# Performance work log

Hardware: AMD Instinct MI355X
Metric: run time of the kernel (lower is better)

## Reference

```python
import jax, jax.numpy as jnp
import numpy as np

# dims
B, S, IN, H = 8, 2048, 512, 512
# biophysical constants (from module defaults / buffers)
DT = 0.1
TAU_M, TAU_ADAPT = 20.0, 100.0
V_REST, V_THRESH, V_RESET = -65.0, -50.0, -65.0
ADAPT_A, ADAPT_B = 0.5, 0.1
E_NA, E_K, E_L = 50.0, -77.0, -54.4
# HH gate initial values (IonicCurrents lazy init)
M0, H0, N0 = 0.05, 0.6, 0.32


def setup_inputs() -> dict:
    key = jax.random.key(0)
    k1, k2 = jax.random.split(key)
    x = jax.random.normal(k1, (B, S, IN), dtype=jnp.float32)
    W = jax.random.normal(k2, (H, IN), dtype=jnp.float32) * 0.01  # SynapticPlasticity.weights
    return {
        "x": x,
        "W": W,
        "g_Na": jnp.float32(120.0),
        "g_K": jnp.float32(36.0),
        "g_L": jnp.float32(0.3),
    }


def reference(x, W, g_Na, g_K, g_L):
    """BiologicalSNNLayer.forward, first call (all internal states at init).

    post_spikes = psp0 = 0 and traces start at 0, so the STDP dw is exactly 0
    on this call; psp = 0*decay + syn_input = syn_input.
    """
    dt = jnp.float32(DT)
    # SynapticPlasticity forward output: F.linear(x, W)
    syn = jnp.einsum("bsi,hi->bsh", x, W)  # [B,S,H]
    psp = syn
    V = psp
    # Hodgkin-Huxley gating: one Euler step from initial gate values
    am = 0.1 * (V + 40.0) / (1.0 - jnp.exp(-(V + 40.0) / 10.0))
    bm = 4.0 * jnp.exp(-(V + 65.0) / 18.0)
    ah = 0.07 * jnp.exp(-(V + 65.0) / 20.0)
    bh = 1.0 / (1.0 + jnp.exp(-(V + 35.0) / 10.0))
    an = 0.01 * (V + 55.0) / (1.0 - jnp.exp(-(V + 55.0) / 10.0))
    bn = 0.125 * jnp.exp(-(V + 65.0) / 80.0)
    m = M0 + dt * (am * (1.0 - M0) - bm * M0)
    h = H0 + dt * (ah * (1.0 - H0) - bh * H0)
    n = N0 + dt * (an * (1.0 - N0) - bn * N0)
    I_ion = (
        g_Na * m ** 3 * h * (V - E_NA)
        + g_K * n ** 4 * (V - E_K)
        + g_L * (V - E_L)
    )
    # Adaptive LIF (all hidden_size neurons share params -> vectorized over last dim)
    I_in = I_ion + psp
    # v0 = V_REST, w0 = 0 -> dv = I_in * dt/tau_m
    v_new = V_REST + I_in * (dt / TAU_M)
    spike = (v_new >= V_THRESH).astype(jnp.float32)
    w_new = (ADAPT_A * (v_new - V_REST) + ADAPT_B * spike) * (dt / TAU_ADAPT)
    v_rs = jnp.where(spike > 0.5, jnp.float32(V_RESET), v_new)
    return spike, v_rs, w_new
```

## Files before the change

kernel.cpp:

```cpp
#include <hip/hip_runtime.h>
#include <hip/hip_bf16.h>
#include <math.h>

typedef __bf16 bf16x4 __attribute__((ext_vector_type(4)));
typedef __bf16 bf16x8 __attribute__((ext_vector_type(8)));
typedef float  f32x4  __attribute__((ext_vector_type(4)));

#define BM 64
#define BN 128
#define BK 64
#define LDST 72
#define TBL_N 1024

#define M_DIM 16384
#define N_DIM 512
#define K_DIM 512

__global__ __launch_bounds__(256, 4)
void snn_fused_kernel(const float* __restrict__ x, const float* __restrict__ W,
                      const float* __restrict__ gNa_p, const float* __restrict__ gK_p,
                      const float* __restrict__ gL_p, float* __restrict__ out)
{
    __shared__ __bf16 sA[BM * LDST];
    __shared__ __bf16 sB[BN * LDST];
    __shared__ float  tbl[TBL_N + 1];

    const int tid = threadIdx.x;

    const int id   = blockIdx.x;
    const int xcd  = id & 7;
    const int slot = id >> 3;
    const int bm   = xcd * 32 + (slot >> 2);
    const int bn   = slot & 3;

    const int c4 = (tid & 15) * 4;
    const int r0 = tid >> 4;

    const float* xBase = x + (long)(bm * BM + r0) * K_DIM + c4;
    const float* wBase = W + (long)(bn * BN + r0) * K_DIM + c4;

    const int wave = tid >> 6;
    const int lane = tid & 63;
    const int wM   = (wave & 1) * 32;
    const int wN   = (wave >> 1) * 64;
    const int lr   = lane & 15;
    const int quad = lane >> 4;

    f32x4 acc[2][4] = {};

    float4 pa[4], pb[8];
    #pragma unroll
    for (int rr = 0; rr < 4; ++rr)
        pa[rr] = *(const float4*)(xBase + (long)rr * 16 * K_DIM);
    #pragma unroll
    for (int rr = 0; rr < 8; ++rr)
        pb[rr] = *(const float4*)(wBase + (long)rr * 16 * K_DIM);

    {
        const float gNa = *gNa_p, gK = *gK_p, gL = *gL_p;
        for (int i = tid; i <= TBL_N; i += 256) {
            const float V = -4.0f + (8.0f / TBL_N) * i;
            const float am = 0.1f * (V + 40.0f) / (1.0f - expf(-(V + 40.0f) * 0.1f));
            const float bm_ = 4.0f * expf(-(V + 65.0f) * (1.0f / 18.0f));
            const float ah = 0.07f * expf(-(V + 65.0f) * 0.05f);
            const float bh = 1.0f / (1.0f + expf(-(V + 35.0f) * 0.1f));
            const float an = 0.01f * (V + 55.0f) / (1.0f - expf(-(V + 55.0f) * 0.1f));
            const float bn_ = 0.125f * expf(-(V + 65.0f) * 0.0125f);
            const float m = 0.05f + 0.1f * (am * 0.95f - bm_ * 0.05f);
            const float h = 0.60f + 0.1f * (ah * 0.40f - bh * 0.60f);
            const float n = 0.32f + 0.1f * (an * 0.68f - bn_ * 0.32f);
            const float I_ion = gNa * m * m * m * h * (V - 50.0f)
                              + gK * (n * n) * (n * n) * (V + 77.0f)
                              + gL * (V + 54.4f);
            tbl[i] = I_ion + V;
        }
    }

    for (int kt = 0; kt < K_DIM; kt += BK) {
        const int ktn = (kt + BK < K_DIM) ? kt + BK : kt;
        const float* xp = xBase + ktn;
        const float* wp = wBase + ktn;

        #pragma unroll
        for (int rr = 0; rr < 4; ++rr) {
            float4 v = pa[rr];
            pa[rr] = *(const float4*)(xp + (long)rr * 16 * K_DIM);
            bf16x4 b = { (__bf16)v.x, (__bf16)v.y, (__bf16)v.z, (__bf16)v.w };
            *(bf16x4*)(&sA[(r0 + rr * 16) * LDST + c4]) = b;
        }
        #pragma unroll
        for (int rr = 0; rr < 8; ++rr) {
            float4 v = pb[rr];
            pb[rr] = *(const float4*)(wp + (long)rr * 16 * K_DIM);
            bf16x4 b = { (__bf16)v.x, (__bf16)v.y, (__bf16)v.z, (__bf16)v.w };
            *(bf16x4*)(&sB[(r0 + rr * 16) * LDST + c4]) = b;
        }
        __syncthreads();

        #pragma unroll
        for (int ks = 0; ks < BK; ks += 32) {
            bf16x8 af[2], bfr[4];
            #pragma unroll
            for (int t = 0; t < 2; ++t)
                af[t]  = *(const bf16x8*)(&sA[(wM + t * 16 + lr) * LDST + ks + quad * 8]);
            #pragma unroll
            for (int t = 0; t < 4; ++t)
                bfr[t] = *(const bf16x8*)(&sB[(wN + t * 16 + lr) * LDST + ks + quad * 8]);
            #pragma unroll
            for (int mt = 0; mt < 2; ++mt)
                #pragma unroll
                for (int nt = 0; nt < 4; ++nt)
                    acc[mt][nt] = __builtin_amdgcn_mfma_f32_16x16x32_bf16(
                        af[mt], bfr[nt], acc[mt][nt], 0, 0, 0);
        }
        __syncthreads();
    }

    float* outS = out;
    float* outV = out + (long)M_DIM * N_DIM;
    float* outW = out + 2L * M_DIM * N_DIM;

    #pragma unroll
    for (int mt = 0; mt < 2; ++mt) {
        #pragma unroll
        for (int i = 0; i < 4; ++i) {
            const long gm = (long)bm * BM + wM + mt * 16 + quad * 4 + i;
            #pragma unroll
            for (int nt = 0; nt < 4; ++nt) {
                const int gn = bn * BN + wN + nt * 16 + lr;
                const float V = acc[mt][nt][i];

                float u = (V + 4.0f) * (TBL_N / 8.0f);
                u = fminf(fmaxf(u, 0.0f), (float)TBL_N - 0.001f);
                const int   iu = (int)u;
                const float f  = u - (float)iu;
                const float t0 = tbl[iu];
                const float t1 = tbl[iu + 1];
                const float I_in = t0 + f * (t1 - t0);

                const float v_new = -65.0f + I_in * 0.005f;
                const float spike = (v_new >= -50.0f) ? 1.0f : 0.0f;
                const float w_new = (0.5f * (v_new + 65.0f) + 0.1f * spike) * 0.001f;
                const float v_rs  = (spike > 0.5f) ? -65.0f : v_new;

                const long idx = gm * N_DIM + gn;
                outS[idx] = spike;
                outV[idx] = v_rs;
                outW[idx] = w_new;
            }
        }
    }
}

extern "C" void kernel_launch(void* const* d_in, const int* in_sizes, int n_in,
                              void* d_out, int out_size, void* d_ws, size_t ws_size,
                              hipStream_t stream) {
    const float* x   = (const float*)d_in[0];
    const float* W   = (const float*)d_in[1];
    const float* gNa = (const float*)d_in[2];
    const float* gK  = (const float*)d_in[3];
    const float* gL  = (const float*)d_in[4];
    float* out = (float*)d_out;

    dim3 grid((M_DIM / BM) * (N_DIM / BN));
    dim3 block(256);
    hipLaunchKernelGGL(snn_fused_kernel, grid, block, 0, stream, x, W, gNa, gK, gL, out);
}
```

Measured before the change: 156.5 us.

## Pre-convert inputs to bf16 and use direct global-to-LDS loads with larger tiles

Adds a separate pass that converts x and W to bf16 in the workspace. The GEMM kernel then streams bf16 tiles straight into LDS with global_load_lds, using an XOR swizzle, and computes a 128x128 tile per block instead of 64x128. The goal is to halve operand traffic inside the GEMM and to drop the register-staged fp32-to-bf16 conversion from the main loop. The cost is an extra launch and a full read of x plus a bf16 write and re-read. The new loop also gives up the register prefetch overlap and keeps a single-buffered sync loop. The old kernel stays as a fallback when the workspace is too small.

```diff
diff --git a/kernel.cpp b/kernel.cpp
--- a/kernel.cpp
+++ b/kernel.cpp
@@ -6,55 +6,52 @@
 typedef __bf16 bf16x8 __attribute__((ext_vector_type(8)));
 typedef float  f32x4  __attribute__((ext_vector_type(4)));
 
-#define BM 64
-#define BN 128
-#define BK 64
-#define LDST 72
-#define TBL_N 1024
-
 #define M_DIM 16384
 #define N_DIM 512
 #define K_DIM 512
-
-__global__ __launch_bounds__(256, 4)
-void snn_fused_kernel(const float* __restrict__ x, const float* __restrict__ W,
-                      const float* __restrict__ gNa_p, const float* __restrict__ gK_p,
-                      const float* __restrict__ gL_p, float* __restrict__ out)
+#define TBL_N 1024
+
+#define X_ELEMS ((long)M_DIM * K_DIM)
+#define W_ELEMS ((long)N_DIM * K_DIM)
+#define WS_NEED ((X_ELEMS + W_ELEMS) * 2)
+
+__global__ __launch_bounds__(256)
+void convert_kernel(const float* __restrict__ x, const float* __restrict__ W,
+                    __bf16* __restrict__ xb, __bf16* __restrict__ wb)
 {
-    __shared__ __bf16 sA[BM * LDST];
-    __shared__ __bf16 sB[BN * LDST];
+    const long XN8 = X_ELEMS / 8;
+    const long T8  = XN8 + W_ELEMS / 8;
+    for (long i = (long)blockIdx.x * 256 + threadIdx.x; i < T8;
+         i += (long)gridDim.x * 256) {
+        const float* src;
+        __bf16* dst;
+        if (i < XN8) { src = x + i * 8;          dst = xb + i * 8; }
+        else         { src = W + (i - XN8) * 8;  dst = wb + (i - XN8) * 8; }
+        float4 a = *(const float4*)src;
+        float4 b = *(const float4*)(src + 4);
+        bf16x8 r;
+        r[0] = (__bf16)a.x; r[1] = (__bf16)a.y; r[2] = (__bf16)a.z; r[3] = (__bf16)a.w;
+        r[4] = (__bf16)b.x; r[5] = (__bf16)b.y; r[6] = (__bf16)b.z; r[7] = (__bf16)b.w;
+        *(bf16x8*)dst = r;
+    }
+}
+
+__device__ inline void gl_lds16(const __bf16* g, __bf16* l) {
+    __builtin_amdgcn_global_load_lds(
+        (const __attribute__((address_space(1))) void*)g,
+        (__attribute__((address_space(3))) void*)l, 16, 0, 0);
+}
+
+__global__ __launch_bounds__(256, 2)
+void gemm_hh_kernel(const __bf16* __restrict__ xb, const __bf16* __restrict__ wb,
+                    const float* __restrict__ gNa_p, const float* __restrict__ gK_p,
+                    const float* __restrict__ gL_p, float* __restrict__ out)
+{
+    __shared__ __bf16 sA[128 * 64];
+    __shared__ __bf16 sB[128 * 64];
     __shared__ float  tbl[TBL_N + 1];
 
     const int tid = threadIdx.x;
-
-    const int id   = blockIdx.x;
-    const int xcd  = id & 7;
-    const int slot = id >> 3;
-    const int bm   = xcd * 32 + (slot >> 2);
-    const int bn   = slot & 3;
-
-    const int c4 = (tid & 15) * 4;
-    const int r0 = tid >> 4;
-
-    const float* xBase = x + (long)(bm * BM + r0) * K_DIM + c4;
-    const float* wBase = W + (long)(bn * BN + r0) * K_DIM + c4;
-
-    const int wave = tid >> 6;
-    const int lane = tid & 63;
-    const int wM   = (wave & 1) * 32;
-    const int wN   = (wave >> 1) * 64;
-    const int lr   = lane & 15;
-    const int quad = lane >> 4;
-
-    f32x4 acc[2][4] = {};
-
-    float4 pa[4], pb[8];
-    #pragma unroll
-    for (int rr = 0; rr < 4; ++rr)
-        pa[rr] = *(const float4*)(xBase + (long)rr * 16 * K_DIM);
-    #pragma unroll
-    for (int rr = 0; rr < 8; ++rr)
-        pb[rr] = *(const float4*)(wBase + (long)rr * 16 * K_DIM);
 
     {
         const float gNa = *gNa_p, gK = *gK_p, gL = *gL_p;
@@ -76,38 +73,48 @@
         }
     }
 
-    for (int kt = 0; kt < K_DIM; kt += BK) {
-        const int ktn = (kt + BK < K_DIM) ? kt + BK : kt;
-        const float* xp = xBase + ktn;
-        const float* wp = wBase + ktn;
-
-        #pragma unroll
-        for (int rr = 0; rr < 4; ++rr) {
-            float4 v = pa[rr];
-            pa[rr] = *(const float4*)(xp + (long)rr * 16 * K_DIM);
-            bf16x4 b = { (__bf16)v.x, (__bf16)v.y, (__bf16)v.z, (__bf16)v.w };
-            *(bf16x4*)(&sA[(r0 + rr * 16) * LDST + c4]) = b;
-        }
-        #pragma unroll
-        for (int rr = 0; rr < 8; ++rr) {
-            float4 v = pb[rr];
-            pb[rr] = *(const float4*)(wp + (long)rr * 16 * K_DIM);
-            bf16x4 b = { (__bf16)v.x, (__bf16)v.y, (__bf16)v.z, (__bf16)v.w };
-            *(bf16x4*)(&sB[(r0 + rr * 16) * LDST + c4]) = b;
+    const int id   = blockIdx.x;
+    const int xcd  = id & 7;
+    const int slot = id >> 3;
+    const int bm   = xcd * 16 + (slot >> 2);
+    const int bn   = slot & 3;
+
+    const int wv = tid >> 6;
+    const int ln = tid & 63;
+    const int lr = ln & 15;
+    const int quad = ln >> 4;
+    const int wM = (wv & 1) * 64;
+    const int wN = (wv >> 1) * 64;
+
+    const int rw  = ln >> 3;
+    const int ch  = ln & 7;
+    const int chx = (ch ^ rw) * 8;
+    const __bf16* aSrc = xb + ((long)bm * 128 + 32 * wv + rw) * K_DIM + chx;
+    const __bf16* bSrc = wb + ((long)bn * 128 + 32 * wv + rw) * K_DIM + chx;
+
+    f32x4 acc[4][4] = {};
+
+    for (int kt = 0; kt < K_DIM; kt += 64) {
+        #pragma unroll
+        for (int j = 0; j < 4; ++j) {
+            gl_lds16(aSrc + (long)(8 * j) * K_DIM + kt, sA + (32 * wv + 8 * j) * 64);
+            gl_lds16(bSrc + (long)(8 * j) * K_DIM + kt, sB + (32 * wv + 8 * j) * 64);
         }
         __syncthreads();
 
         #pragma unroll
-        for (int ks = 0; ks < BK; ks += 32) {
-            bf16x8 af[2], bfr[4];
-            #pragma unroll
-            for (int t = 0; t < 2; ++t)
-                af[t]  = *(const bf16x8*)(&sA[(wM + t * 16 + lr) * LDST + ks + quad * 8]);
-            #pragma unroll
-            for (int t = 0; t < 4; ++t)
-                bfr[t] = *(const bf16x8*)(&sB[(wN + t * 16 + lr) * LDST + ks + quad * 8]);
-            #pragma unroll
-            for (int mt = 0; mt < 2; ++mt)
+        for (int kk = 0; kk < 2; ++kk) {
+            bf16x8 af[4], bfr[4];
+            #pragma unroll
+            for (int t = 0; t < 4; ++t) {
+                const int ra = wM + t * 16 + lr;
+                const int rb = wN + t * 16 + lr;
+                const int cidx = quad + 4 * kk;
+                af[t]  = *(const bf16x8*)(sA + ra * 64 + ((cidx ^ (lr & 7)) * 8));
+                bfr[t] = *(const bf16x8*)(sB + rb * 64 + ((cidx ^ (lr & 7)) * 8));
+            }
+            #pragma unroll
+            for (int mt = 0; mt < 4; ++mt)
                 #pragma unroll
                 for (int nt = 0; nt < 4; ++nt)
                     acc[mt][nt] = __builtin_amdgcn_mfma_f32_16x16x32_bf16(
@@ -121,13 +128,13 @@
     float* outW = out + 2L * M_DIM * N_DIM;
 
     #pragma unroll
-    for (int mt = 0; mt < 2; ++mt) {
+    for (int mt = 0; mt < 4; ++mt) {
         #pragma unroll
         for (int i = 0; i < 4; ++i) {
-            const long gm = (long)bm * BM + wM + mt * 16 + quad * 4 + i;
+            const long gm = (long)bm * 128 + wM + mt * 16 + quad * 4 + i;
             #pragma unroll
             for (int nt = 0; nt < 4; ++nt) {
-                const int gn = bn * BN + wN + nt * 16 + lr;
+                const int gn = bn * 128 + wN + nt * 16 + lr;
                 const float V = acc[mt][nt][i];
 
                 float u = (V + 4.0f) * (TBL_N / 8.0f);
@@ -147,6 +154,129 @@
                 outS[idx] = spike;
                 outV[idx] = v_rs;
                 outW[idx] = w_new;
+            }
+        }
+    }
+}
+
+#define BMf 64
+#define BNf 128
+#define LDSTf 72
+__global__ __launch_bounds__(256, 4)
+void snn_fallback_kernel(const float* __restrict__ x, const float* __restrict__ W,
+                         const float* __restrict__ gNa_p, const float* __restrict__ gK_p,
+                         const float* __restrict__ gL_p, float* __restrict__ out)
+{
+    __shared__ __bf16 sA[BMf * LDSTf];
+    __shared__ __bf16 sB[BNf * LDSTf];
+    __shared__ float  tbl[TBL_N + 1];
+
+    const int tid = threadIdx.x;
+    const int id   = blockIdx.x;
+    const int xcd  = id & 7;
+    const int slot = id >> 3;
+    const int bm   = xcd * 32 + (slot >> 2);
+    const int bn   = slot & 3;
+
+    const int c4 = (tid & 15) * 4;
+    const int r0 = tid >> 4;
+    const float* xBase = x + (long)(bm * BMf + r0) * K_DIM + c4;
+    const float* wBase = W + (long)(bn * BNf + r0) * K_DIM + c4;
+
+    const int wave = tid >> 6;
+    const int lane = tid & 63;
+    const int wM   = (wave & 1) * 32;
+    const int wN   = (wave >> 1) * 64;
+    const int lr   = lane & 15;
+    const int quad = lane >> 4;
+
+    f32x4 acc[2][4] = {};
+    float4 pa[4], pb[8];
+    #pragma unroll
+    for (int rr = 0; rr < 4; ++rr) pa[rr] = *(const float4*)(xBase + (long)rr * 16 * K_DIM);
+    #pragma unroll
+    for (int rr = 0; rr < 8; ++rr) pb[rr] = *(const float4*)(wBase + (long)rr * 16 * K_DIM);
+
+    {
+        const float gNa = *gNa_p, gK = *gK_p, gL = *gL_p;
+        for (int i = tid; i <= TBL_N; i += 256) {
+            const float V = -4.0f + (8.0f / TBL_N) * i;
+            const float am = 0.1f * (V + 40.0f) / (1.0f - expf(-(V + 40.0f) * 0.1f));
+            const float bm_ = 4.0f * expf(-(V + 65.0f) * (1.0f / 18.0f));
+            const float ah = 0.07f * expf(-(V + 65.0f) * 0.05f);
+            const float bh = 1.0f / (1.0f + expf(-(V + 35.0f) * 0.1f));
+            const float an = 0.01f * (V + 55.0f) / (1.0f - expf(-(V + 55.0f) * 0.1f));
+            const float bn_ = 0.125f * expf(-(V + 65.0f) * 0.0125f);
+            const float m = 0.05f + 0.1f * (am * 0.95f - bm_ * 0.05f);
+            const float h = 0.60f + 0.1f * (ah * 0.40f - bh * 0.60f);
+            const float n = 0.32f + 0.1f * (an * 0.68f - bn_ * 0.32f);
+            tbl[i] = gNa * m * m * m * h * (V - 50.0f)
+                   + gK * (n * n) * (n * n) * (V + 77.0f)
+                   + gL * (V + 54.4f) + V;
+        }
+    }
+
+    for (int kt = 0; kt < K_DIM; kt += 64) {
+        const int ktn = (kt + 64 < K_DIM) ? kt + 64 : kt;
+        const float* xp = xBase + ktn;
+        const float* wp = wBase + ktn;
+        #pragma unroll
+        for (int rr = 0; rr < 4; ++rr) {
+            float4 v = pa[rr];
+            pa[rr] = *(const float4*)(xp + (long)rr * 16 * K_DIM);
+            bf16x4 b = { (__bf16)v.x, (__bf16)v.y, (__bf16)v.z, (__bf16)v.w };
+            *(bf16x4*)(&sA[(r0 + rr * 16) * LDSTf + c4]) = b;
+        }
+        #pragma unroll
+        for (int rr = 0; rr < 8; ++rr) {
+            float4 v = pb[rr];
+            pb[rr] = *(const float4*)(wp + (long)rr * 16 * K_DIM);
+            bf16x4 b = { (__bf16)v.x, (__bf16)v.y, (__bf16)v.z, (__bf16)v.w };
+            *(bf16x4*)(&sB[(r0 + rr * 16) * LDSTf + c4]) = b;
+        }
+        __syncthreads();
+        #pragma unroll
+        for (int ks = 0; ks < 64; ks += 32) {
+            bf16x8 af[2], bfr[4];
+            #pragma unroll
+            for (int t = 0; t < 2; ++t)
+                af[t]  = *(const bf16x8*)(&sA[(wM + t * 16 + lr) * LDSTf + ks + quad * 8]);
+            #pragma unroll
+            for (int t = 0; t < 4; ++t)
+                bfr[t] = *(const bf16x8*)(&sB[(wN + t * 16 + lr) * LDSTf + ks + quad * 8]);
+            #pragma unroll
+            for (int mt = 0; mt < 2; ++mt)
+                #pragma unroll
+                for (int nt = 0; nt < 4; ++nt)
+                    acc[mt][nt] = __builtin_amdgcn_mfma_f32_16x16x32_bf16(
+                        af[mt], bfr[nt], acc[mt][nt], 0, 0, 0);
+        }
+        __syncthreads();
+    }
+
+    float* outS = out;
+    float* outV = out + (long)M_DIM * N_DIM;
+    float* outW = out + 2L * M_DIM * N_DIM;
+    #pragma unroll
+    for (int mt = 0; mt < 2; ++mt) {
+        #pragma unroll
+        for (int i = 0; i < 4; ++i) {
+            const long gm = (long)bm * BMf + wM + mt * 16 + quad * 4 + i;
+            #pragma unroll
+            for (int nt = 0; nt < 4; ++nt) {
+                const int gn = bn * BNf + wN + nt * 16 + lr;
+                const float V = acc[mt][nt][i];
+                float u = (V + 4.0f) * (TBL_N / 8.0f);
+                u = fminf(fmaxf(u, 0.0f), (float)TBL_N - 0.001f);
+                const int   iu = (int)u;
+                const float f  = u - (float)iu;
+                const float I_in = tbl[iu] + f * (tbl[iu + 1] - tbl[iu]);
+                const float v_new = -65.0f + I_in * 0.005f;
+                const float spike = (v_new >= -50.0f) ? 1.0f : 0.0f;
+                const float w_new = (0.5f * (v_new + 65.0f) + 0.1f * spike) * 0.001f;
+                const float v_rs  = (spike > 0.5f) ? -65.0f : v_new;
+                const long idx = gm * N_DIM + gn;
+                outS[idx] = spike; outV[idx] = v_rs; outW[idx] = w_new;
             }
         }
     }
@@ -162,7 +292,14 @@
     const float* gL  = (const float*)d_in[4];
     float* out = (float*)d_out;
 
-    dim3 grid((M_DIM / BM) * (N_DIM / BN));
-    dim3 block(256);
-    hipLaunchKernelGGL(snn_fused_kernel, grid, block, 0, stream, x, W, gNa, gK, gL, out);
-}
+    if (ws_size >= (size_t)WS_NEED) {
+        __bf16* xb = (__bf16*)d_ws;
+        __bf16* wb = xb + X_ELEMS;
+        hipLaunchKernelGGL(convert_kernel, dim3(1024), dim3(256), 0, stream, x, W, xb, wb);
+        hipLaunchKernelGGL(gemm_hh_kernel, dim3(512), dim3(256), 0, stream,
+                           xb, wb, gNa, gK, gL, out);
+    } else {
+        hipLaunchKernelGGL(snn_fallback_kernel, dim3(1024), dim3(256), 0, stream,
+                           x, W, gNa, gK, gL, out);
+    }
+}
```

After: 149.0 us. 1.05x faster.
